# Optimization experiments

Measured on AMD Instinct MI355X. Metric: run time of the kernel, lower is better.

Reference implementation:

```python
import jax, jax.numpy as jnp
import numpy as np

B, N, L, H = 8, 2048, 1280, 160
GAMMA = 1.0  # fixed buffer, gamma_init_value=1, not trainable


def setup_inputs() -> dict:
    key = jax.random.key(0)
    ks = jax.random.split(key, 7)
    s_in = 1.0 / np.sqrt(L)  # conv1d default init scale (approx; randn used for testing)
    return {
        "x": jax.random.normal(ks[0], (B, N, L), dtype=jnp.float32),
        "Wq": jax.random.normal(ks[1], (H, L), dtype=jnp.float32) * s_in,
        "bq": jax.random.normal(ks[2], (H,), dtype=jnp.float32) * s_in,
        "Wk": jax.random.normal(ks[3], (H, L), dtype=jnp.float32) * s_in,
        "bk": jax.random.normal(ks[4], (H,), dtype=jnp.float32) * s_in,
        "Wv": jax.random.normal(ks[5], (L, L), dtype=jnp.float32) * s_in,
        "bv": jax.random.normal(ks[6], (L,), dtype=jnp.float32) * s_in,
    }


def reference(x, Wq, bq, Wk, bk, Wv, bv):
    # 1x1 Conv1d on x.permute(0,2,1) == per-token linear projection
    q = jnp.einsum("bnl,hl->bnh", x, Wq) + bq          # [B,N,H]
    k = jnp.einsum("bnl,hl->bnh", x, Wk) + bk          # [B,N,H]
    v = jnp.einsum("bnl,ml->bnm", x, Wv) + bv          # [B,N,L]
    energy = jnp.einsum("bih,bjh->bij", q, k)          # [B,N,N]
    attn = jax.nn.softmax(energy, axis=-1)
    out = jnp.einsum("bij,bjm->bim", attn, v)          # [B,N,L]
    return GAMMA * out + x                              # [B,N,L]
```

## Files before the change

kernel.cpp:

```cpp
#include <hip/hip_runtime.h>

#define BB 8
#define NN 2048
#define LL 1280
#define HH 160
#define BN (BB*NN)
#define NO (2*HH + LL)
#define SHIFT 40.0f

typedef __attribute__((ext_vector_type(8))) short short8;
typedef __attribute__((ext_vector_type(4))) float floatx4;

__device__ __forceinline__ unsigned short f2bf(float f) {
    unsigned int u = __builtin_bit_cast(unsigned int, f);
    u = (u + 0x7FFFu + ((u >> 16) & 1u)) >> 16;
    return (unsigned short)u;
}
__device__ __forceinline__ float bf2f(unsigned short h) {
    unsigned int u = ((unsigned int)h) << 16;
    return __builtin_bit_cast(float, u);
}
__device__ __forceinline__ void split2(float f, unsigned short& hi, unsigned short& lo) {
    hi = f2bf(f);
    lo = f2bf(f - bf2f(hi));
}


__device__ __forceinline__ void gl16(const unsigned short* g, unsigned short* l) {
    __builtin_amdgcn_global_load_lds(
        (const __attribute__((address_space(1))) unsigned int*)g,
        (__attribute__((address_space(3))) unsigned int*)l, 16, 0, 0);
}

__global__ __launch_bounds__(256) void cast_w(
    const float* __restrict__ Wq, const float* __restrict__ Wk, const float* __restrict__ Wv,
    unsigned short* __restrict__ wqk_h, unsigned short* __restrict__ wqk_l,
    unsigned short* __restrict__ wv)
{
    int o = blockIdx.x;
    if (o < 2*HH) {
        const float* src = (o < HH) ? (Wq + (size_t)o * LL) : (Wk + (size_t)(o - HH) * LL);
        unsigned short* dh = wqk_h + (size_t)(o >> 4) * 20480 + (o & 15) * 8;
        unsigned short* dl = wqk_l + (size_t)(o >> 4) * 20480 + (o & 15) * 8;
        for (int c = threadIdx.x; c < LL; c += 256) {
            unsigned short h, l;
            split2(src[c], h, l);
            unsigned off = (unsigned)(c >> 5) * 512 + ((c >> 3) & 3) * 128 + (c & 7);
            dh[off] = h; dl[off] = l;
        }
    } else {
        int f = o - 2*HH;
        const float* src = Wv + (size_t)f * LL;
        unsigned short* dstF = wv + (size_t)(f >> 4) * 20480 + (f & 15) * 8;
        for (int c = threadIdx.x * 4; c < LL; c += 256 * 4) {
            float4 v = *(const float4*)(src + c);
            ushort4 u;
            u.x = f2bf(v.x); u.y = f2bf(v.y); u.z = f2bf(v.z); u.w = f2bf(v.w);
            *(ushort4*)(dstF + (size_t)(c >> 5) * 512 + ((c >> 3) & 3) * 128 + (c & 7)) = u;
        }
    }
}

__global__ __launch_bounds__(256) void cast_x(
    const float* __restrict__ x,
    unsigned short* __restrict__ xh, unsigned short* __restrict__ xl)
{
    const int g   = blockIdx.x;
    const int tid = threadIdx.x;
    const float* src = x + (size_t)(g * 16 + (tid & 15)) * LL + ((tid >> 4) & 3) * 8;
    unsigned short* dsth = xh + (size_t)g * 20480 + tid * 8;
    unsigned short* dstl = xl + (size_t)g * 20480 + tid * 8;
    const int ks0 = tid >> 6;
    #pragma unroll
    for (int it = 0; it < 10; it++) {
        int k0 = (it * 4 + ks0) * 32;
        float4 f0 = *(const float4*)(src + k0);
        float4 f1 = *(const float4*)(src + k0 + 4);
        float fv[8] = {f0.x, f0.y, f0.z, f0.w, f1.x, f1.y, f1.z, f1.w};
        short8 h8, l8;
        #pragma unroll
        for (int i = 0; i < 8; i++) {
            unsigned short hh, lll;
            split2(fv[i], hh, lll);
            h8[i] = (short)hh; l8[i] = (short)lll;
        }
        *(short8*)(dsth + it * 2048) = h8;
        *(short8*)(dstl + it * 2048) = l8;
    }
}

__global__ __launch_bounds__(256, 2) void proj_qk(
    const unsigned short* __restrict__ xh, const unsigned short* __restrict__ xl,
    const unsigned short* __restrict__ wh, const unsigned short* __restrict__ wl,
    const float* __restrict__ bq, const float* __restrict__ bk,
    unsigned short* __restrict__ qh, unsigned short* __restrict__ ql,
    unsigned short* __restrict__ kh, unsigned short* __restrict__ kl)
{
    const int mg0 = blockIdx.x * 2;
    const int tid = threadIdx.x;
    const int wave = tid >> 6, lane = tid & 63;
    const int l15 = lane & 15, l4 = lane >> 4;

    const unsigned aBase = (unsigned)mg0 * 20480u + lane * 8;
    const unsigned bBase = (unsigned)(wave * 5) * 20480u + lane * 8;

    floatx4 acc[2][5] = {};

    #pragma unroll 2
    for (int ks = 0; ks < 40; ks++) {
        const unsigned ko = (unsigned)ks * 512u;
        short8 ah[2], al[2], bh[5], bl[5];
        #pragma unroll
        for (int mf = 0; mf < 2; mf++) {
            ah[mf] = *(const short8*)(xh + aBase + mf * 20480u + ko);
            al[mf] = *(const short8*)(xl + aBase + mf * 20480u + ko);
        }
        #pragma unroll
        for (int nf = 0; nf < 5; nf++) {
            bh[nf] = *(const short8*)(wh + bBase + nf * 20480u + ko);
            bl[nf] = *(const short8*)(wl + bBase + nf * 20480u + ko);
        }
        #pragma unroll
        for (int mf = 0; mf < 2; mf++)
            #pragma unroll
            for (int nf = 0; nf < 5; nf++) {
                acc[mf][nf] = __builtin_amdgcn_mfma_f32_16x16x32_bf16(ah[mf], bh[nf], acc[mf][nf], 0, 0, 0);
                acc[mf][nf] = __builtin_amdgcn_mfma_f32_16x16x32_bf16(al[mf], bh[nf], acc[mf][nf], 0, 0, 0);
                acc[mf][nf] = __builtin_amdgcn_mfma_f32_16x16x32_bf16(ah[mf], bl[nf], acc[mf][nf], 0, 0, 0);
            }
    }

    #pragma unroll
    for (int nf = 0; nf < 5; nf++) {
        int o = wave * 80 + nf * 16 + l15;
        bool isQ = (o < HH);
        float bias = isQ ? bq[o] : bk[o - HH];
        int oo = isQ ? o : (o - HH);
        unsigned short* dh = isQ ? qh : kh;
        unsigned short* dl = isQ ? ql : kl;
        unsigned ob = (unsigned)(oo >> 5) * 512u + ((oo >> 3) & 3) * 128u + (oo & 7);
        #pragma unroll
        for (int mf = 0; mf < 2; mf++) {
            unsigned fa0 = (unsigned)(mg0 + mf) * 2560u + ob + (l4 * 4) * 8u;
            #pragma unroll
            for (int r = 0; r < 4; r++) {
                float val = acc[mf][nf][r] + bias;
                unsigned short vh, vl;
                split2(val, vh, vl);
                dh[fa0 + r * 8] = vh;
                dl[fa0 + r * 8] = vl;
            }
        }
    }
}

__global__ __launch_bounds__(256, 3) void proj_v(
    const unsigned short* __restrict__ xh, const unsigned short* __restrict__ wv,
    const float* __restrict__ bv, unsigned short* __restrict__ vt)
{
    __shared__ __align__(16) unsigned short Sm[3 * 8192];

    const int bid = blockIdx.x;
    const int xcd = bid & 7;
    const int q   = bid >> 3;
    const int mt  = xcd * 16 + q / 10;
    const int ft  = q % 10;
    const int m0 = mt * 128;
    const int f0 = ft * 128;

    const int tid = threadIdx.x;
    const int wave = tid >> 6, lane = tid & 63;
    const int l15 = lane & 15, l4 = lane >> 4;
    const int wm = wave >> 1, wn = wave & 1;

    const unsigned short* AF = xh + (size_t)(m0 >> 4) * 20480;
    const unsigned short* BF = wv + (size_t)(f0 >> 4) * 20480;

    const int sp0 = tid, sp1 = 256 + tid;
    const unsigned sa0 = (unsigned)(sp0 >> 6) * 20480u + (sp0 & 63) * 8;
    const unsigned sa1 = (unsigned)(sp1 >> 6) * 20480u + (sp1 & 63) * 8;

    floatx4 acc[4][4] = {};

    auto STAGE = [&](int slot, int ks) {
        unsigned short* A  = Sm + slot * 8192;
        unsigned short* Bs = A + 4096;
        const unsigned ko = (unsigned)ks * 512u;
        gl16(AF + sa0 + ko, A  + sp0 * 8);
        gl16(BF + sa0 + ko, Bs + sp0 * 8);
        gl16(AF + sa1 + ko, A  + sp1 * 8);
        gl16(BF + sa1 + ko, Bs + sp1 * 8);
    };

    auto COMPUTE = [&](int slot) {
        const unsigned short* A  = Sm + slot * 8192;
        const unsigned short* Bs = A + 4096;
        short8 a[4], bb[4];
        #pragma unroll
        for (int mf = 0; mf < 4; mf++)
            a[mf] = *(const short8*)(A + ((wm * 4 + mf) * 64 + lane) * 8);
        #pragma unroll
        for (int nf = 0; nf < 4; nf++)
            bb[nf] = *(const short8*)(Bs + ((wn * 4 + nf) * 64 + lane) * 8);
        __builtin_amdgcn_s_setprio(1);
        #pragma unroll
        for (int mf = 0; mf < 4; mf++)
            #pragma unroll
            for (int nf = 0; nf < 4; nf++)
                acc[mf][nf] = __builtin_amdgcn_mfma_f32_16x16x32_bf16(a[mf], bb[nf], acc[mf][nf], 0, 0, 0);
        __builtin_amdgcn_s_setprio(0);
    };

    STAGE(0, 0); STAGE(1, 1); STAGE(2, 2);

    int s = 0;
    for (int kt = 0; kt < 37; ++kt) {
        asm volatile("s_waitcnt vmcnt(8)" ::: "memory");
        asm volatile("s_barrier" ::: "memory");
        COMPUTE(s);
        asm volatile("s_barrier" ::: "memory");
        STAGE(s, kt + 3);
        s = (s == 2) ? 0 : s + 1;
    }
    asm volatile("s_waitcnt vmcnt(8)" ::: "memory");
    asm volatile("s_barrier" ::: "memory");
    COMPUTE(s); s = (s == 2) ? 0 : s + 1;
    asm volatile("s_waitcnt vmcnt(4)" ::: "memory");
    asm volatile("s_barrier" ::: "memory");
    COMPUTE(s); s = (s == 2) ? 0 : s + 1;
    asm volatile("s_waitcnt vmcnt(0)" ::: "memory");
    asm volatile("s_barrier" ::: "memory");
    COMPUTE(s);

    const int b    = m0 >> 11;
    const int tokb = (m0 & 2047) + wm * 64;
    unsigned short* vtB = vt + (size_t)b * LL * NN;
    float bvv[4];
    #pragma unroll
    for (int nf = 0; nf < 4; nf++)
        bvv[nf] = bv[f0 + wn * 64 + nf * 16 + l15];

    #pragma unroll
    for (int mf = 0; mf < 4; mf++)
        #pragma unroll
        for (int nf = 0; nf < 4; nf++) {
            int f   = f0 + wn * 64 + nf * 16 + l15;
            int tok = tokb + mf * 16 + l4 * 4;
            ushort4 u;
            u.x = f2bf(acc[mf][nf][0] + bvv[nf]);
            u.y = f2bf(acc[mf][nf][1] + bvv[nf]);
            u.z = f2bf(acc[mf][nf][2] + bvv[nf]);
            u.w = f2bf(acc[mf][nf][3] + bvv[nf]);
            *(ushort4*)(vtB + (size_t)(f >> 4) * 32768 + (tok >> 5) * 512
                        + ((tok >> 3) & 3) * 128 + (f & 15) * 8 + (tok & 7)) = u;
        }
}

__global__ __launch_bounds__(512, 2) void s_exp(
    const unsigned short* __restrict__ qhp, const unsigned short* __restrict__ qlp,
    const unsigned short* __restrict__ khp, const unsigned short* __restrict__ klp,
    unsigned short* __restrict__ P, float* __restrict__ Lsum)
{
    __shared__ float sums[8][64];
    const int bid = blockIdx.x;
    const int b   = bid & 7;
    const int i0  = (bid >> 3) * 64;
    const int tid = threadIdx.x;
    const int wave = tid >> 6, lane = tid & 63;
    const int l15 = lane & 15, l4 = lane >> 4;

    short8 aqh[4][5], aql[4][5];
    #pragma unroll
    for (int rt = 0; rt < 4; rt++) {
        const size_t rowb = (size_t)((b * NN + i0 + rt * 16) >> 4) * 2560 + lane * 8;
        #pragma unroll
        for (int ks = 0; ks < 5; ks++) {
            aqh[rt][ks] = *(const short8*)&qhp[rowb + ks * 512];
            aql[rt][ks] = *(const short8*)&qlp[rowb + ks * 512];
        }
    }

    float sr[4][4] = {};
    unsigned short* Pb = P + (size_t)b * NN * NN + (size_t)(i0 >> 4) * 32768;

    for (int c0 = 0; c0 < NN; c0 += 512) {
        const int jb = c0 + wave * 64;
        #pragma unroll
        for (int ct = 0; ct < 4; ct++) {
            const int tok0 = jb + ct * 16;
            const int tok  = tok0 + l15;
            const size_t kbase = (size_t)((b * NN + tok0) >> 4) * 2560 + lane * 8;
            floatx4 a[4] = {{0,0,0,0},{0,0,0,0},{0,0,0,0},{0,0,0,0}};
            #pragma unroll
            for (int ks = 0; ks < 5; ks++) {
                short8 bh = *(const short8*)&khp[kbase + ks * 512];
                short8 bl = *(const short8*)&klp[kbase + ks * 512];
                #pragma unroll
                for (int rt = 0; rt < 4; rt++) {
                    a[rt] = __builtin_amdgcn_mfma_f32_16x16x32_bf16(aqh[rt][ks], bh, a[rt], 0, 0, 0);
                    a[rt] = __builtin_amdgcn_mfma_f32_16x16x32_bf16(aql[rt][ks], bh, a[rt], 0, 0, 0);
                    a[rt] = __builtin_amdgcn_mfma_f32_16x16x32_bf16(aqh[rt][ks], bl, a[rt], 0, 0, 0);
                }
            }
            const size_t tbase = (size_t)(tok >> 5) * 512 + ((tok >> 3) & 3) * 128 + (tok & 7);
            #pragma unroll
            for (int rt = 0; rt < 4; rt++)
                #pragma unroll
                for (int r = 0; r < 4; r++) {
                    float p = __expf(a[rt][r] - SHIFT);
                    Pb[tbase + (size_t)rt * 32768 + (l4 * 4 + r) * 8] = f2bf(p);
                    sr[rt][r] += p;
                }
        }
    }

    #pragma unroll
    for (int rt = 0; rt < 4; rt++)
        #pragma unroll
        for (int r = 0; r < 4; r++) {
            float v = sr[rt][r];
            v += __shfl_xor(v, 1);
            v += __shfl_xor(v, 2);
            v += __shfl_xor(v, 4);
            v += __shfl_xor(v, 8);
            if (l15 == 0) sums[wave][rt * 16 + l4 * 4 + r] = v;
        }
    __syncthreads();
    if (tid < 64) {
        float s = 0.f;
        #pragma unroll
        for (int w = 0; w < 8; w++) s += sums[w][tid];
        Lsum[(size_t)b * NN + i0 + tid] = s;
    }
}

__global__ __launch_bounds__(256, 3) void pv_gemm(
    const unsigned short* __restrict__ P, const unsigned short* __restrict__ vt,
    const float* __restrict__ Lsum,
    const float* __restrict__ x, float* __restrict__ out)
{
    __shared__ __align__(16) unsigned short Sm[3 * 8192];

    const int p0 = blockIdx.x;
    const int b  = p0 & 7;
    const int t  = p0 >> 3;
    const int n0 = (t % 10) * 128;
    const int m0 = (t / 10) * 128;

    const int tid = threadIdx.x;
    const int wave = tid >> 6, lane = tid & 63;
    const int l15 = lane & 15, l4 = lane >> 4;
    const int wm = wave >> 1, wn = wave & 1;

    const unsigned short* PbF = P  + (size_t)b * NN * NN + (size_t)(m0 >> 4) * 32768;
    const unsigned short* VbF = vt + (size_t)b * LL * NN + (size_t)(n0 >> 4) * 32768;

    const int sp0 = tid, sp1 = 256 + tid;
    const unsigned sa0 = (unsigned)(sp0 >> 6) * 32768u + (sp0 & 63) * 8;
    const unsigned sa1 = (unsigned)(sp1 >> 6) * 32768u + (sp1 & 63) * 8;

    floatx4 acc[4][4] = {};

    auto STAGE = [&](int slot, int ks) {
        unsigned short* A  = Sm + slot * 8192;
        unsigned short* Bs = A + 4096;
        const unsigned ko = (unsigned)ks * 512u;
        gl16(PbF + sa0 + ko, A  + sp0 * 8);
        gl16(VbF + sa0 + ko, Bs + sp0 * 8);
        gl16(PbF + sa1 + ko, A  + sp1 * 8);
        gl16(VbF + sa1 + ko, Bs + sp1 * 8);
    };

    auto COMPUTE = [&](int slot) {
        const unsigned short* A  = Sm + slot * 8192;
        const unsigned short* Bs = A + 4096;
        short8 a[4], bb[4];
        #pragma unroll
        for (int mf = 0; mf < 4; mf++)
            a[mf] = *(const short8*)(A + ((wm * 4 + mf) * 64 + lane) * 8);
        #pragma unroll
        for (int nf = 0; nf < 4; nf++)
            bb[nf] = *(const short8*)(Bs + ((wn * 4 + nf) * 64 + lane) * 8);
        __builtin_amdgcn_s_setprio(1);
        #pragma unroll
        for (int mf = 0; mf < 4; mf++)
            #pragma unroll
            for (int nf = 0; nf < 4; nf++)
                acc[mf][nf] = __builtin_amdgcn_mfma_f32_16x16x32_bf16(a[mf], bb[nf], acc[mf][nf], 0, 0, 0);
        __builtin_amdgcn_s_setprio(0);
    };

    STAGE(0, 0); STAGE(1, 1); STAGE(2, 2);

    int s = 0;
    for (int kt = 0; kt < 61; ++kt) {
        asm volatile("s_waitcnt vmcnt(8)" ::: "memory");
        asm volatile("s_barrier" ::: "memory");
        COMPUTE(s);
        asm volatile("s_barrier" ::: "memory");
        STAGE(s, kt + 3);
        s = (s == 2) ? 0 : s + 1;
    }
    asm volatile("s_waitcnt vmcnt(8)" ::: "memory");
    asm volatile("s_barrier" ::: "memory");
    COMPUTE(s); s = (s == 2) ? 0 : s + 1;
    asm volatile("s_waitcnt vmcnt(4)" ::: "memory");
    asm volatile("s_barrier" ::: "memory");
    COMPUTE(s); s = (s == 2) ? 0 : s + 1;
    asm volatile("s_waitcnt vmcnt(0)" ::: "memory");
    asm volatile("s_barrier" ::: "memory");
    COMPUTE(s);

    float linv[4][4];
    #pragma unroll
    for (int mf = 0; mf < 4; mf++)
        #pragma unroll
        for (int r = 0; r < 4; r++)
            linv[mf][r] = 1.0f / Lsum[(size_t)b * NN + m0 + wm * 64 + mf * 16 + l4 * 4 + r];

    #pragma unroll
    for (int mf = 0; mf < 4; mf++)
        #pragma unroll
        for (int nf = 0; nf < 4; nf++)
            #pragma unroll
            for (int r = 0; r < 4; r++) {
                int row = m0 + wm * 64 + mf * 16 + l4 * 4 + r;
                int col = n0 + wn * 64 + nf * 16 + l15;
                size_t idx = ((size_t)b * NN + row) * LL + col;
                out[idx] = acc[mf][nf][r] * linv[mf][r] + x[idx];
            }
}

extern "C" void kernel_launch(void* const* d_in, const int* in_sizes, int n_in,
                              void* d_out, int out_size, void* d_ws, size_t ws_size,
                              hipStream_t stream) {
    const float* x  = (const float*)d_in[0];
    const float* Wq = (const float*)d_in[1];
    const float* bq = (const float*)d_in[2];
    const float* Wk = (const float*)d_in[3];
    const float* bk = (const float*)d_in[4];
    const float* Wv = (const float*)d_in[5];
    const float* bv = (const float*)d_in[6];
    float* out = (float*)d_out;

    unsigned short* wqk_h = (unsigned short*)d_ws;
    unsigned short* wqk_l = wqk_h + (size_t)2*HH * LL;
    unsigned short* wv    = wqk_l + (size_t)2*HH * LL;
    unsigned short* qh    = wv    + (size_t)LL * LL;
    unsigned short* ql    = qh    + (size_t)BN * HH;
    unsigned short* kh    = ql    + (size_t)BN * HH;
    unsigned short* kl    = kh    + (size_t)BN * HH;
    unsigned short* vt    = kl    + (size_t)BN * HH;
    unsigned short* P     = vt    + (size_t)BB * LL * NN;
    float*          Lsum  = (float*)(P + (size_t)BB * NN * NN);
    unsigned short* xh    = P;
    unsigned short* xl    = vt;

    cast_w<<<dim3(NO), dim3(256), 0, stream>>>(Wq, Wk, Wv, wqk_h, wqk_l, wv);

    cast_x<<<dim3(BN / 16), dim3(256), 0, stream>>>(x, xh, xl);

    proj_qk<<<dim3(BN / 32), dim3(256), 0, stream>>>(
        xh, xl, wqk_h, wqk_l, bq, bk, qh, ql, kh, kl);

    proj_v<<<dim3(1280), dim3(256), 0, stream>>>(xh, wv, bv, vt);

    s_exp<<<dim3(256), dim3(512), 0, stream>>>(qh, ql, kh, kl, P, Lsum);

    pv_gemm<<<dim3(1280), dim3(256), 0, stream>>>(P, vt, Lsum, x, out);
}
```

Measured before the change: 425.8 us.

## Switch PV GEMM to 32x32x16 MFMA with matching P and V tile layouts

Rewrites the P·V GEMM to use 32x32x16 bf16 MFMA instructions with 2x2 accumulators per wave instead of 4x4 16x16x32 tiles. The global layouts of P (written by s_exp) and V^T (written by the projection kernel) change to 32-row groups so the LDS staging loads map directly onto the larger MFMA operand format. The intent is fewer MFMA issues and LDS reads per k-step and higher matrix-core throughput. The epilogue is rewritten for the 32x32 accumulator row mapping, which changes the store access pattern for out/x.

```diff
diff --git a/kernel.cpp b/kernel.cpp
--- a/kernel.cpp
+++ b/kernel.cpp
@@ -10,6 +10,7 @@
 
 typedef __attribute__((ext_vector_type(8))) short short8;
 typedef __attribute__((ext_vector_type(4))) float floatx4;
+typedef __attribute__((ext_vector_type(16))) float floatx16;
 
 __device__ __forceinline__ unsigned short f2bf(float f) {
     unsigned int u = __builtin_bit_cast(unsigned int, f);
@@ -244,15 +245,16 @@
     for (int mf = 0; mf < 4; mf++)
         #pragma unroll
         for (int nf = 0; nf < 4; nf++) {
-            int f   = f0 + wn * 64 + nf * 16 + l15;
-            int tok = tokb + mf * 16 + l4 * 4;
+            int fgrp = (f0 >> 5) + wn * 2 + (nf >> 1);
+            int fin  = (nf & 1) * 16 + l15;
+            size_t addr = (size_t)fgrp * 65536 + (size_t)((tokb >> 4) + mf) * 512
+                        + ((l4 >> 1) * 32 + fin) * 8 + (l4 & 1) * 4;
             ushort4 u;
             u.x = f2bf(acc[mf][nf][0] + bvv[nf]);
             u.y = f2bf(acc[mf][nf][1] + bvv[nf]);
             u.z = f2bf(acc[mf][nf][2] + bvv[nf]);
             u.w = f2bf(acc[mf][nf][3] + bvv[nf]);
-            *(ushort4*)(vtB + (size_t)(f >> 4) * 32768 + (tok >> 5) * 512
-                        + ((tok >> 3) & 3) * 128 + (f & 15) * 8 + (tok & 7)) = u;
+            *(ushort4*)(vtB + addr) = u;
         }
 }
 
@@ -281,14 +283,13 @@
     }
 
     float sr[4][4] = {};
-    unsigned short* Pb = P + (size_t)b * NN * NN + (size_t)(i0 >> 4) * 32768;
+    unsigned short* Pb = P + (size_t)b * NN * NN + (size_t)(i0 >> 5) * 65536;
 
     for (int c0 = 0; c0 < NN; c0 += 512) {
         const int jb = c0 + wave * 64;
         #pragma unroll
         for (int ct = 0; ct < 4; ct++) {
             const int tok0 = jb + ct * 16;
-            const int tok  = tok0 + l15;
             const size_t kbase = (size_t)((b * NN + tok0) >> 4) * 2560 + lane * 8;
             floatx4 a[4] = {{0,0,0,0},{0,0,0,0},{0,0,0,0},{0,0,0,0}};
             #pragma unroll
@@ -302,13 +303,14 @@
                     a[rt] = __builtin_amdgcn_mfma_f32_16x16x32_bf16(aqh[rt][ks], bl, a[rt], 0, 0, 0);
                 }
             }
-            const size_t tbase = (size_t)(tok >> 5) * 512 + ((tok >> 3) & 3) * 128 + (tok & 7);
+            const size_t tb32 = (size_t)(tok0 >> 4) * 512 + (l15 >> 3) * 256 + (l15 & 7);
             #pragma unroll
             for (int rt = 0; rt < 4; rt++)
                 #pragma unroll
                 for (int r = 0; r < 4; r++) {
                     float p = __expf(a[rt][r] - SHIFT);
-                    Pb[tbase + (size_t)rt * 32768 + (l4 * 4 + r) * 8] = f2bf(p);
+                    Pb[tb32 + (size_t)(rt >> 1) * 65536
+                       + ((rt & 1) * 16 + l4 * 4 + r) * 8] = f2bf(p);
                     sr[rt][r] += p;
                 }
         }
@@ -349,22 +351,22 @@
 
     const int tid = threadIdx.x;
     const int wave = tid >> 6, lane = tid & 63;
-    const int l15 = lane & 15, l4 = lane >> 4;
+    const int l31 = lane & 31, l5 = lane >> 5;
     const int wm = wave >> 1, wn = wave & 1;
 
-    const unsigned short* PbF = P  + (size_t)b * NN * NN + (size_t)(m0 >> 4) * 32768;
-    const unsigned short* VbF = vt + (size_t)b * LL * NN + (size_t)(n0 >> 4) * 32768;
+    const unsigned short* PbF = P  + (size_t)b * NN * NN + (size_t)(m0 >> 5) * 65536;
+    const unsigned short* VbF = vt + (size_t)b * LL * NN + (size_t)(n0 >> 5) * 65536;
 
     const int sp0 = tid, sp1 = 256 + tid;
-    const unsigned sa0 = (unsigned)(sp0 >> 6) * 32768u + (sp0 & 63) * 8;
-    const unsigned sa1 = (unsigned)(sp1 >> 6) * 32768u + (sp1 & 63) * 8;
-
-    floatx4 acc[4][4] = {};
+    const unsigned sa0 = (unsigned)(sp0 >> 7) * 65536u + (sp0 & 127) * 8;
+    const unsigned sa1 = (unsigned)(sp1 >> 7) * 65536u + (sp1 & 127) * 8;
+
+    floatx16 acc[2][2] = {};
 
     auto STAGE = [&](int slot, int ks) {
         unsigned short* A  = Sm + slot * 8192;
         unsigned short* Bs = A + 4096;
-        const unsigned ko = (unsigned)ks * 512u;
+        const unsigned ko = (unsigned)ks * 1024u;
         gl16(PbF + sa0 + ko, A  + sp0 * 8);
         gl16(VbF + sa0 + ko, Bs + sp0 * 8);
         gl16(PbF + sa1 + ko, A  + sp1 * 8);
@@ -374,19 +376,22 @@
     auto COMPUTE = [&](int slot) {
         const unsigned short* A  = Sm + slot * 8192;
         const unsigned short* Bs = A + 4096;
-        short8 a[4], bb[4];
-        #pragma unroll
-        for (int mf = 0; mf < 4; mf++)
-            a[mf] = *(const short8*)(A + ((wm * 4 + mf) * 64 + lane) * 8);
-        #pragma unroll
-        for (int nf = 0; nf < 4; nf++)
-            bb[nf] = *(const short8*)(Bs + ((wn * 4 + nf) * 64 + lane) * 8);
+        short8 a[2][2], bb[2][2];
+        #pragma unroll
+        for (int i = 0; i < 2; i++)
+            #pragma unroll
+            for (int h = 0; h < 2; h++) {
+                a[i][h]  = *(const short8*)(A  + ((2 * wm + i) * 2 + h) * 512 + lane * 8);
+                bb[i][h] = *(const short8*)(Bs + ((2 * wn + i) * 2 + h) * 512 + lane * 8);
+            }
         __builtin_amdgcn_s_setprio(1);
         #pragma unroll
-        for (int mf = 0; mf < 4; mf++)
-            #pragma unroll
-            for (int nf = 0; nf < 4; nf++)
-                acc[mf][nf] = __builtin_amdgcn_mfma_f32_16x16x32_bf16(a[mf], bb[nf], acc[mf][nf], 0, 0, 0);
+        for (int i = 0; i < 2; i++)
+            #pragma unroll
+            for (int j = 0; j < 2; j++) {
+                acc[i][j] = __builtin_amdgcn_mfma_f32_32x32x16_bf16(a[i][0], bb[j][0], acc[i][j], 0, 0, 0);
+                acc[i][j] = __builtin_amdgcn_mfma_f32_32x32x16_bf16(a[i][1], bb[j][1], acc[i][j], 0, 0, 0);
+            }
         __builtin_amdgcn_s_setprio(0);
     };
 
@@ -411,23 +416,25 @@
     asm volatile("s_barrier" ::: "memory");
     COMPUTE(s);
 
-    float linv[4][4];
-    #pragma unroll
-    for (int mf = 0; mf < 4; mf++)
-        #pragma unroll
-        for (int r = 0; r < 4; r++)
-            linv[mf][r] = 1.0f / Lsum[(size_t)b * NN + m0 + wm * 64 + mf * 16 + l4 * 4 + r];
-
-    #pragma unroll
-    for (int mf = 0; mf < 4; mf++)
-        #pragma unroll
-        for (int nf = 0; nf < 4; nf++)
-            #pragma unroll
-            for (int r = 0; r < 4; r++) {
-                int row = m0 + wm * 64 + mf * 16 + l4 * 4 + r;
-                int col = n0 + wn * 64 + nf * 16 + l15;
+    float linv[2][16];
+    #pragma unroll
+    for (int i = 0; i < 2; i++)
+        #pragma unroll
+        for (int reg = 0; reg < 16; reg++) {
+            int row = m0 + wm * 64 + i * 32 + (reg & 3) + 8 * (reg >> 2) + 4 * l5;
+            linv[i][reg] = 1.0f / Lsum[(size_t)b * NN + row];
+        }
+
+    #pragma unroll
+    for (int i = 0; i < 2; i++)
+        #pragma unroll
+        for (int j = 0; j < 2; j++)
+            #pragma unroll
+            for (int reg = 0; reg < 16; reg++) {
+                int row = m0 + wm * 64 + i * 32 + (reg & 3) + 8 * (reg >> 2) + 4 * l5;
+                int col = n0 + wn * 64 + j * 32 + l31;
                 size_t idx = ((size_t)b * NN + row) * LL + col;
-                out[idx] = acc[mf][nf][r] * linv[mf][r] + x[idx];
+                out[idx] = acc[i][j][reg] * linv[i][reg] + x[idx];
             }
 }
 
```

Result: slower. 466.4 us (+9.5%).

## Use two waves per PV block with 64x128 per-wave tiles

Applied to the files above, without the earlier changes.

The PV GEMM block drops from four waves (each computing 64x64) to two waves (each computing 64x128). The block tile stays 128x128, so each wave loads 8 global chunks per stage instead of 4, and the wait counts are adjusted to match. The goal is a better MFMA-to-LDS-read ratio, since each A fragment is reused across 8 B fragments, and fewer waves per barrier. The cost is twice the accumulator registers per wave and fewer waves available to hide latency.

```diff
diff --git a/kernel.cpp b/kernel.cpp
--- a/kernel.cpp
+++ b/kernel.cpp
@@ -334,7 +334,7 @@
     }
 }
 
-__global__ __launch_bounds__(256, 3) void pv_gemm(
+__global__ __launch_bounds__(128, 2) void pv_gemm(
     const unsigned short* __restrict__ P, const unsigned short* __restrict__ vt,
     const float* __restrict__ Lsum,
     const float* __restrict__ x, float* __restrict__ out)
@@ -348,45 +348,48 @@
     const int m0 = (t / 10) * 128;
 
     const int tid = threadIdx.x;
-    const int wave = tid >> 6, lane = tid & 63;
+    const int wm  = tid >> 6, lane = tid & 63;
     const int l15 = lane & 15, l4 = lane >> 4;
-    const int wm = wave >> 1, wn = wave & 1;
 
     const unsigned short* PbF = P  + (size_t)b * NN * NN + (size_t)(m0 >> 4) * 32768;
     const unsigned short* VbF = vt + (size_t)b * LL * NN + (size_t)(n0 >> 4) * 32768;
 
-    const int sp0 = tid, sp1 = 256 + tid;
-    const unsigned sa0 = (unsigned)(sp0 >> 6) * 32768u + (sp0 & 63) * 8;
-    const unsigned sa1 = (unsigned)(sp1 >> 6) * 32768u + (sp1 & 63) * 8;
-
-    floatx4 acc[4][4] = {};
+    unsigned sa[4], dof[4];
+    #pragma unroll
+    for (int i = 0; i < 4; i++) {
+        int p = i * 128 + tid;
+        sa[i]  = (unsigned)(p >> 6) * 32768u + (p & 63) * 8;
+        dof[i] = (unsigned)p * 8;
+    }
+
+    floatx4 acc[4][8] = {};
 
     auto STAGE = [&](int slot, int ks) {
         unsigned short* A  = Sm + slot * 8192;
         unsigned short* Bs = A + 4096;
         const unsigned ko = (unsigned)ks * 512u;
-        gl16(PbF + sa0 + ko, A  + sp0 * 8);
-        gl16(VbF + sa0 + ko, Bs + sp0 * 8);
-        gl16(PbF + sa1 + ko, A  + sp1 * 8);
-        gl16(VbF + sa1 + ko, Bs + sp1 * 8);
+        #pragma unroll
+        for (int i = 0; i < 4; i++) {
+            gl16(PbF + sa[i] + ko, A  + dof[i]);
+            gl16(VbF + sa[i] + ko, Bs + dof[i]);
+        }
     };
 
     auto COMPUTE = [&](int slot) {
         const unsigned short* A  = Sm + slot * 8192;
         const unsigned short* Bs = A + 4096;
-        short8 a[4], bb[4];
+        short8 a[4];
         #pragma unroll
         for (int mf = 0; mf < 4; mf++)
             a[mf] = *(const short8*)(A + ((wm * 4 + mf) * 64 + lane) * 8);
-        #pragma unroll
-        for (int nf = 0; nf < 4; nf++)
-            bb[nf] = *(const short8*)(Bs + ((wn * 4 + nf) * 64 + lane) * 8);
         __builtin_amdgcn_s_setprio(1);
         #pragma unroll
-        for (int mf = 0; mf < 4; mf++)
-            #pragma unroll
-            for (int nf = 0; nf < 4; nf++)
-                acc[mf][nf] = __builtin_amdgcn_mfma_f32_16x16x32_bf16(a[mf], bb[nf], acc[mf][nf], 0, 0, 0);
+        for (int nf = 0; nf < 8; nf++) {
+            short8 bb = *(const short8*)(Bs + (nf * 64 + lane) * 8);
+            #pragma unroll
+            for (int mf = 0; mf < 4; mf++)
+                acc[mf][nf] = __builtin_amdgcn_mfma_f32_16x16x32_bf16(a[mf], bb, acc[mf][nf], 0, 0, 0);
+        }
         __builtin_amdgcn_s_setprio(0);
     };
 
@@ -394,17 +397,17 @@
 
     int s = 0;
     for (int kt = 0; kt < 61; ++kt) {
-        asm volatile("s_waitcnt vmcnt(8)" ::: "memory");
+        asm volatile("s_waitcnt vmcnt(16)" ::: "memory");
         asm volatile("s_barrier" ::: "memory");
         COMPUTE(s);
         asm volatile("s_barrier" ::: "memory");
         STAGE(s, kt + 3);
         s = (s == 2) ? 0 : s + 1;
     }
+    asm volatile("s_waitcnt vmcnt(16)" ::: "memory");
+    asm volatile("s_barrier" ::: "memory");
+    COMPUTE(s); s = (s == 2) ? 0 : s + 1;
     asm volatile("s_waitcnt vmcnt(8)" ::: "memory");
-    asm volatile("s_barrier" ::: "memory");
-    COMPUTE(s); s = (s == 2) ? 0 : s + 1;
-    asm volatile("s_waitcnt vmcnt(4)" ::: "memory");
     asm volatile("s_barrier" ::: "memory");
     COMPUTE(s); s = (s == 2) ? 0 : s + 1;
     asm volatile("s_waitcnt vmcnt(0)" ::: "memory");
@@ -421,11 +424,11 @@
     #pragma unroll
     for (int mf = 0; mf < 4; mf++)
         #pragma unroll
-        for (int nf = 0; nf < 4; nf++)
+        for (int nf = 0; nf < 8; nf++)
             #pragma unroll
             for (int r = 0; r < 4; r++) {
                 int row = m0 + wm * 64 + mf * 16 + l4 * 4 + r;
-                int col = n0 + wn * 64 + nf * 16 + l15;
+                int col = n0 + nf * 16 + l15;
                 size_t idx = ((size_t)b * NN + row) * LL + col;
                 out[idx] = acc[mf][nf][r] * linv[mf][r] + x[idx];
             }
@@ -467,5 +470,5 @@
 
     s_exp<<<dim3(256), dim3(512), 0, stream>>>(qh, ql, kh, kl, P, Lsum);
 
-    pv_gemm<<<dim3(1280), dim3(256), 0, stream>>>(P, vt, Lsum, x, out);
-}
+    pv_gemm<<<dim3(1280), dim3(128), 0, stream>>>(P, vt, Lsum, x, out);
+}
```

Measured after the change: 432.8 us. Within noise of the previous version (+1.6%).

## Load V operand directly into registers in pv_gemm, bypassing LDS

Applied to the files above, without the earlier changes.

In the P·V GEMM, the V (B operand) tiles no longer go through shared memory. Each wave loads its MFMA B fragments straight from global memory into registers, double-buffered one k-step ahead, and only the P tiles stay in the three-slot LDS ring. This halves the LDS footprint and removes the LDS reads for B. In exchange, the two waves that share a column half each fetch the same V data from global memory, and the vmcnt waits now depend on the mix of register and LDS loads in flight.

```diff
diff --git a/kernel.cpp b/kernel.cpp
--- a/kernel.cpp
+++ b/kernel.cpp
@@ -339,7 +339,7 @@
     const float* __restrict__ Lsum,
     const float* __restrict__ x, float* __restrict__ out)
 {
-    __shared__ __align__(16) unsigned short Sm[3 * 8192];
+    __shared__ __align__(16) unsigned short Sm[3 * 4096];
 
     const int p0 = blockIdx.x;
     const int b  = p0 & 7;
@@ -359,54 +359,69 @@
     const unsigned sa0 = (unsigned)(sp0 >> 6) * 32768u + (sp0 & 63) * 8;
     const unsigned sa1 = (unsigned)(sp1 >> 6) * 32768u + (sp1 & 63) * 8;
 
+    const unsigned bb0 = (unsigned)(wn * 4) * 32768u + lane * 8;
+
     floatx4 acc[4][4] = {};
 
     auto STAGE = [&](int slot, int ks) {
-        unsigned short* A  = Sm + slot * 8192;
-        unsigned short* Bs = A + 4096;
+        unsigned short* A = Sm + slot * 4096;
         const unsigned ko = (unsigned)ks * 512u;
-        gl16(PbF + sa0 + ko, A  + sp0 * 8);
-        gl16(VbF + sa0 + ko, Bs + sp0 * 8);
-        gl16(PbF + sa1 + ko, A  + sp1 * 8);
-        gl16(VbF + sa1 + ko, Bs + sp1 * 8);
+        gl16(PbF + sa0 + ko, A + sp0 * 8);
+        gl16(PbF + sa1 + ko, A + sp1 * 8);
     };
 
+    short8 bP[4], bN[4];
+    auto LOADB = [&](short8* dst, int ks) {
+        const unsigned ko = (unsigned)ks * 512u;
+        #pragma unroll
+        for (int nf = 0; nf < 4; nf++)
+            dst[nf] = *(const short8*)(VbF + bb0 + nf * 32768u + ko);
+    };
+
     auto COMPUTE = [&](int slot) {
-        const unsigned short* A  = Sm + slot * 8192;
-        const unsigned short* Bs = A + 4096;
-        short8 a[4], bb[4];
+        const unsigned short* A = Sm + slot * 4096;
+        short8 a[4];
         #pragma unroll
         for (int mf = 0; mf < 4; mf++)
             a[mf] = *(const short8*)(A + ((wm * 4 + mf) * 64 + lane) * 8);
-        #pragma unroll
-        for (int nf = 0; nf < 4; nf++)
-            bb[nf] = *(const short8*)(Bs + ((wn * 4 + nf) * 64 + lane) * 8);
         __builtin_amdgcn_s_setprio(1);
         #pragma unroll
         for (int mf = 0; mf < 4; mf++)
             #pragma unroll
             for (int nf = 0; nf < 4; nf++)
-                acc[mf][nf] = __builtin_amdgcn_mfma_f32_16x16x32_bf16(a[mf], bb[nf], acc[mf][nf], 0, 0, 0);
+                acc[mf][nf] = __builtin_amdgcn_mfma_f32_16x16x32_bf16(a[mf], bP[nf], acc[mf][nf], 0, 0, 0);
         __builtin_amdgcn_s_setprio(0);
     };
 
     STAGE(0, 0); STAGE(1, 1); STAGE(2, 2);
+    LOADB(bP, 0);
 
     int s = 0;
     for (int kt = 0; kt < 61; ++kt) {
-        asm volatile("s_waitcnt vmcnt(8)" ::: "memory");
+        asm volatile("s_waitcnt vmcnt(4)" ::: "memory");
         asm volatile("s_barrier" ::: "memory");
+        LOADB(bN, kt + 1);
         COMPUTE(s);
         asm volatile("s_barrier" ::: "memory");
         STAGE(s, kt + 3);
+        #pragma unroll
+        for (int nf = 0; nf < 4; nf++) bP[nf] = bN[nf];
         s = (s == 2) ? 0 : s + 1;
     }
-    asm volatile("s_waitcnt vmcnt(8)" ::: "memory");
-    asm volatile("s_barrier" ::: "memory");
-    COMPUTE(s); s = (s == 2) ? 0 : s + 1;
     asm volatile("s_waitcnt vmcnt(4)" ::: "memory");
     asm volatile("s_barrier" ::: "memory");
-    COMPUTE(s); s = (s == 2) ? 0 : s + 1;
+    LOADB(bN, 62);
+    COMPUTE(s);
+    #pragma unroll
+    for (int nf = 0; nf < 4; nf++) bP[nf] = bN[nf];
+    s = (s == 2) ? 0 : s + 1;
+    asm volatile("s_waitcnt vmcnt(2)" ::: "memory");
+    asm volatile("s_barrier" ::: "memory");
+    LOADB(bN, 63);
+    COMPUTE(s);
+    #pragma unroll
+    for (int nf = 0; nf < 4; nf++) bP[nf] = bN[nf];
+    s = (s == 2) ? 0 : s + 1;
     asm volatile("s_waitcnt vmcnt(0)" ::: "memory");
     asm volatile("s_barrier" ::: "memory");
     COMPUTE(s);
```

Result: no change. 431.7 us (+1.4%).
